# Kernel tuning notes

Hardware: AMD Instinct MI355X
Metric: run time of the kernel (lower is better)

The kernel has to match this reference:

```python
import jax, jax.numpy as jnp
import numpy as np

K = 3       # kernel_size
RATE = 2    # dilation rate
NH = 8      # num_heads
EPS = 1e-5  # InstanceNorm eps


def _conv1x1(x, W, b):
    # x: [B,C,H,W], W: [O,C], b: [O]
    return jnp.einsum('bchw,oc->bohw', x, W) + b[None, :, None, None]


def _inorm(x):
    mu = jnp.mean(x, axis=(2, 3), keepdims=True)
    var = jnp.var(x, axis=(2, 3), keepdims=True)
    return (x - mu) / jnp.sqrt(var + EPS)


def _extract_patches(x):
    # dilated KxK patches, stride 1, 'same' grid -> [B, C, K*K, H, W]
    B, C, H, W = x.shape
    pad = RATE * (K - 1) // 2
    xp = jnp.pad(x, ((0, 0), (0, 0), (pad, pad), (pad, pad)))
    taps = [xp[:, :, i * RATE:i * RATE + H, j * RATE:j * RATE + W]
            for i in range(K) for j in range(K)]
    return jnp.stack(taps, axis=2)


def setup_inputs() -> dict:
    key = jax.random.key(0)
    ks = jax.random.split(key, 8)
    B, C, H, W, A = 1, 64, 64, 64, 128
    features = jax.random.normal(ks[0], (B, C, H, W), jnp.float32)
    masks = jax.random.uniform(ks[1], (B, 1, H, W), jnp.float32)
    s_in = 1.0 / np.sqrt(C).astype(np.float32)
    Wq = jax.random.normal(ks[2], (A, C), jnp.float32) * s_in
    bq = jnp.zeros((A,), jnp.float32)
    Wk = jax.random.normal(ks[3], (A, C), jnp.float32) * s_in
    bk = jnp.zeros((A,), jnp.float32)
    Wo = jax.random.normal(ks[4], (C, C), jnp.float32) * s_in
    bo = jnp.zeros((C,), jnp.float32)
    return dict(features=features, masks=masks, Wq=Wq, bq=bq,
                Wk=Wk, bk=bk, Wo=Wo, bo=bo)


def reference(features, masks, Wq, bq, Wk, bk, Wo, bo):
    B, C, H, W = features.shape
    A = Wq.shape[0]
    hc = A // NH
    L = H * W
    KK = K * K

    m = (masks > 0.5).astype(features.dtype)          # 1 = hole
    f_masked = features * m
    f_unmasked = features * (1.0 - m)

    q = jax.nn.relu(_inorm(_conv1x1(f_masked, Wq, bq)))    # [B,A,H,W]
    k = jax.nn.relu(_inorm(_conv1x1(f_unmasked, Wk, bk)))  # [B,A,H,W]

    # per-head dilated patch banks: [B,NH,hc*KK,L]
    qp = _extract_patches(q).reshape(B, NH, hc * KK, L)
    kp = _extract_patches(k).reshape(B, NH, hc * KK, L)

    # patch-correlation attention per head: [B,NH,L,L]
    attn = jax.nn.softmax(jnp.einsum('bndq,bndk->bnqk', qp, kp), axis=-1)

    # value patch bank from unmasked features: [B,C*KK,L]
    vp = _extract_patches(f_unmasked).reshape(B, C * KK, L)

    # sample value patches: [B,NH,L,C*KK]
    sampled = jnp.einsum('bnqk,bdk->bnqd', attn, vp)

    # fold: average the KK taps per channel, then average over heads
    attended = sampled.reshape(B, NH, L, C, KK).mean(axis=4).mean(axis=1)  # [B,L,C]
    attended = attended.transpose(0, 2, 1).reshape(B, C, H, W)

    return jax.nn.relu(_inorm(_conv1x1(attended, Wo, bo)))
```

## Files before the change

kernel.cpp:

```cpp
#include <hip/hip_runtime.h>
#include <hip/hip_bf16.h>


#define LL 4096
#define CC 64
#define AA 128
#define NH_ 8
#define KSTR 144
#define LOG2E 1.44269504088896340736f

typedef _Float16 half8 __attribute__((ext_vector_type(8)));
typedef float floatx4 __attribute__((ext_vector_type(4)));
typedef int intx4 __attribute__((ext_vector_type(4)));

__device__ __forceinline__ float fexp2(float x) {
    float r;
    asm("v_exp_f32 %0, %1" : "=v"(r) : "v"(x));
    return r;
}

__global__ __launch_bounds__(256) void prep_kernel(
    const float* __restrict__ feat,
    const float* __restrict__ masks,
    const float* __restrict__ Wq, const float* __restrict__ bq,
    const float* __restrict__ Wk, const float* __restrict__ bk,
    _Float16* __restrict__ q_act, _Float16* __restrict__ k_act,
    _Float16* __restrict__ vb)
{
    const int tid = threadIdx.x;
    const int b = blockIdx.x;
    __shared__ float sW[CC];
    __shared__ float sm[8];

    if (b >= 2 * AA) {
        int c = b - 2 * AA;
        for (int p = 0; p < 16; ++p) {
            int l = p * 256 + tid;
            int y = l >> 6, x = l & 63;
            float s = 0.f;
            for (int ty = 0; ty < 3; ++ty) {
                int yy = y + 2 * (ty - 1);
                if (yy < 0 || yy > 63) continue;
                for (int tx = 0; tx < 3; ++tx) {
                    int xx = x + 2 * (tx - 1);
                    if (xx < 0 || xx > 63) continue;
                    int ll = yy * 64 + xx;
                    float hole = masks[ll] > 0.5f ? 1.f : 0.f;
                    s += feat[c * LL + ll] * (1.f - hole);
                }
            }
            vb[c * LL + l] = (_Float16)(s * (1.f / 9.f));
        }
        return;
    }

    const int a = b & (AA - 1);
    const int sel = b >> 7;
    const float* Wrow = (sel ? Wk : Wq) + a * CC;
    const float bias = sel ? bk[a] : bq[a];
    if (tid < CC) sW[tid] = Wrow[tid];
    __syncthreads();

    float acc[16];
#pragma unroll
    for (int p = 0; p < 16; ++p) acc[p] = 0.f;
    for (int c = 0; c < CC; ++c) {
        float wc = sW[c];
        const float* fr = feat + (size_t)c * LL + tid;
#pragma unroll
        for (int p = 0; p < 16; ++p) acc[p] += wc * fr[p * 256];
    }

    float vals[16];
    float s1 = 0.f, s2 = 0.f;
#pragma unroll
    for (int p = 0; p < 16; ++p) {
        int l = p * 256 + tid;
        float hole = masks[l] > 0.5f ? 1.f : 0.f;
        float mf = sel ? (1.f - hole) : hole;
        float v = acc[p] * mf + bias;
        vals[p] = v; s1 += v; s2 += v * v;
    }
    for (int off = 32; off; off >>= 1) {
        s1 += __shfl_down(s1, off, 64);
        s2 += __shfl_down(s2, off, 64);
    }
    int wv = tid >> 6, ln = tid & 63;
    if (ln == 0) { sm[wv * 2] = s1; sm[wv * 2 + 1] = s2; }
    __syncthreads();
    s1 = sm[0] + sm[2] + sm[4] + sm[6];
    s2 = sm[1] + sm[3] + sm[5] + sm[7];
    float mu = s1 * (1.f / LL);
    float inv = rsqrtf(s2 * (1.f / LL) - mu * mu + 1e-5f);

    const float oscale = sel ? 1.f : LOG2E;
    _Float16* act = (sel ? k_act : q_act) + (size_t)a * LL;
#pragma unroll
    for (int p = 0; p < 16; ++p) {
        int l = p * 256 + tid;
        float v = (vals[p] - mu) * inv;
        act[l] = (_Float16)(v > 0.f ? v * oscale : 0.f);
    }
}

__global__ __launch_bounds__(256) void build_kp(
    const _Float16* __restrict__ k_act, _Float16* __restrict__ kp)
{
    const int n = blockIdx.x, y = blockIdx.y;
    const int tid = threadIdx.x;
    const _Float16* ka = k_act + (size_t)n * 16 * LL;
    _Float16* base = kp + ((size_t)n * LL + y * 64) * KSTR;
#pragma unroll
    for (int i = 0; i < 5; ++i) {
        int idx = tid + i * 256;
        if (idx < 64 * 18) {
            int x = idx / 18, c18 = idx - x * 18;
            half8 v8;
#pragma unroll
            for (int j = 0; j < 8; ++j) {
                int d = c18 * 8 + j;
                int ah = d / 9, t = d - ah * 9;
                int ty = t / 3, tx = t - ty * 3;
                int yy = y + 2 * (ty - 1);
                int xx = x + 2 * (tx - 1);
                _Float16 v = (_Float16)0.f;
                if (yy >= 0 && yy <= 63 && xx >= 0 && xx <= 63)
                    v = ka[ah * LL + yy * 64 + xx];
                v8[j] = v;
            }
            *(half8*)(base + (size_t)idx * 8) = v8;
        }
    }
}

__global__ __launch_bounds__(256, 2) void attn_kernel(
    const _Float16* __restrict__ q_act, const _Float16* __restrict__ kp,
    const _Float16* __restrict__ vb,
    _Float16* __restrict__ Opart, float* __restrict__ ml)
{
    const int qt2 = blockIdx.x, n = blockIdx.y, h = blockIdx.z;
    const int jt0 = h * 32;
    const int tid = threadIdx.x;
    const int w = tid >> 6, lane = tid & 63;
    const int l15 = lane & 15, quad = lane >> 4;

    __shared__ __align__(16) _Float16 Bk[2][64 * KSTR + 16];
    __shared__ __align__(16) _Float16 Vt[2][64 * 64];

    if (tid < 32) Bk[tid >> 4][64 * KSTR + (tid & 15)] = (_Float16)0.f;

    const _Float16* kpn = kp + (size_t)n * LL * KSTR;
    const uint4* vbu = (const uint4*)vb;

    const int vc0 = tid >> 3, ve0 = tid & 7;
    const int vc1 = vc0 + 32, ve1 = ve0;
    const int vs0 = vc0 * 8 + (ve0 ^ (vc0 & 7));
    const int vs1 = vc1 * 8 + (ve1 ^ (vc1 & 7));

    auto issue_bk = [&](int jt, _Float16* dst) {
        const char* tile = (const char*)(kpn + (size_t)jt * 64 * KSTR) + (lane << 4);
        for (int c = w; c < 18; c += 4) {
            __builtin_amdgcn_global_load_lds(
                (const __attribute__((address_space(1))) void*)(tile + c * 1024),
                (__attribute__((address_space(3))) void*)(dst + c * 512),
                16, 0, 0);
        }
    };

    half8 afrag[2][5];
    {
        const _Float16* qa = q_act + (size_t)n * 16 * LL;
        const int x = w * 16 + l15;
#pragma unroll
        for (int rs = 0; rs < 2; ++rs) {
            const int y = qt2 * 2 + rs;
#pragma unroll
            for (int ks = 0; ks < 5; ++ks) {
#pragma unroll
                for (int j = 0; j < 8; ++j) {
                    int d = ks * 32 + quad * 8 + j;
                    _Float16 v = (_Float16)0.f;
                    if (d < 144) {
                        int ah = d / 9, t = d - ah * 9;
                        int ty = t / 3, tx = t - ty * 3;
                        int yy = y + 2 * (ty - 1);
                        int xx = x + 2 * (tx - 1);
                        if (yy >= 0 && yy <= 63 && xx >= 0 && xx <= 63)
                            v = qa[ah * LL + yy * 64 + xx];
                    }
                    afrag[rs][ks][j] = v;
                }
            }
        }
    }

    floatx4 accO[2][4];
    float mrow[2], lrow[2];
#pragma unroll
    for (int rs = 0; rs < 2; ++rs) {
        mrow[rs] = -1e30f; lrow[rs] = 0.f;
#pragma unroll
        for (int i = 0; i < 4; ++i) accO[rs][i] = (floatx4){0.f, 0.f, 0.f, 0.f};
    }

    const int aLo = (((quad & 1) << 5) + l15) << 2;
    const int aHi = aLo + 64;
    const bool selHi = (quad >> 1) != 0;

    uint4 vreg[2];
    issue_bk(jt0, Bk[0]);
    vreg[0] = vbu[vc0 * (LL / 8) + jt0 * 8 + ve0];
    vreg[1] = vbu[vc1 * (LL / 8) + jt0 * 8 + ve1];

    int cur = 0;
    for (int it = 0; it < 32; ++it) {
        {
            uint4* vd = (uint4*)Vt[cur];
            vd[vs0] = vreg[0];
            vd[vs1] = vreg[1];
        }

        __syncthreads();

        if (it < 31) {
            const int jn = jt0 + it + 1;
            issue_bk(jn, Bk[cur ^ 1]);
            vreg[0] = vbu[vc0 * (LL / 8) + jn * 8 + ve0];
            vreg[1] = vbu[vc1 * (LL / 8) + jn * 8 + ve1];
        }

        const _Float16* bk = Bk[cur];
        const _Float16* vt = Vt[cur];

        floatx4 accS[2][4];
#pragma unroll
        for (int rs = 0; rs < 2; ++rs)
#pragma unroll
            for (int i = 0; i < 4; ++i) accS[rs][i] = (floatx4){0.f, 0.f, 0.f, 0.f};
        __builtin_amdgcn_s_setprio(1);
        for (int ks = 0; ks < 5; ++ks) {
#pragma unroll
            for (int nt = 0; nt < 4; ++nt) {
                half8 bfr = *(const half8*)(bk + (nt * 16 + l15) * KSTR + ks * 32 + quad * 8);
                accS[0][nt] = __builtin_amdgcn_mfma_f32_16x16x32_f16(bfr, afrag[0][ks], accS[0][nt], 0, 0, 0);
                accS[1][nt] = __builtin_amdgcn_mfma_f32_16x16x32_f16(bfr, afrag[1][ks], accS[1][nt], 0, 0, 0);
            }
        }
        __builtin_amdgcn_s_setprio(0);

        half8 pfr[2][2];
#pragma unroll
        for (int rs = 0; rs < 2; ++rs) {
            float t0 = fmaxf(fmaxf(accS[rs][0][0], accS[rs][0][1]), fmaxf(accS[rs][0][2], accS[rs][0][3]));
            float t1 = fmaxf(fmaxf(accS[rs][1][0], accS[rs][1][1]), fmaxf(accS[rs][1][2], accS[rs][1][3]));
            float t2 = fmaxf(fmaxf(accS[rs][2][0], accS[rs][2][1]), fmaxf(accS[rs][2][2], accS[rs][2][3]));
            float t3 = fmaxf(fmaxf(accS[rs][3][0], accS[rs][3][1]), fmaxf(accS[rs][3][2], accS[rs][3][3]));
            float tm = fmaxf(fmaxf(t0, t1), fmaxf(t2, t3));
            if (!__all(tm <= mrow[rs] + 3.0f)) {
                tm = fmaxf(tm, __shfl_xor(tm, 16, 64));
                tm = fmaxf(tm, __shfl_xor(tm, 32, 64));
                float mn = fmaxf(mrow[rs], tm);
                float alpha = fexp2(mrow[rs] - mn);
                mrow[rs] = mn;
                lrow[rs] *= alpha;
                float af[4];
#pragma unroll
                for (int r = 0; r < 4; ++r) af[r] = __shfl(alpha, quad * 4 + r, 16);
#pragma unroll
                for (int nt = 0; nt < 4; ++nt)
#pragma unroll
                    for (int r = 0; r < 4; ++r) accO[rs][nt][r] *= af[r];
            }
            float rsum = 0.f;
#pragma unroll
            for (int nt = 0; nt < 4; ++nt)
#pragma unroll
                for (int r = 0; r < 4; ++r) {
                    float pv = fexp2(accS[rs][nt][r] - mrow[rs]);
                    accS[rs][nt][r] = pv;
                    rsum += pv;
                }
            lrow[rs] += rsum;

            int pkw[4][2];
#pragma unroll
            for (int nt = 0; nt < 4; ++nt)
#pragma unroll
                for (int rp = 0; rp < 2; ++rp) {
                    auto hp = __builtin_amdgcn_cvt_pkrtz(accS[rs][nt][2 * rp],
                                                         accS[rs][nt][2 * rp + 1]);
                    pkw[nt][rp] = __builtin_bit_cast(int, hp);
                }
#pragma unroll
            for (int ks2 = 0; ks2 < 2; ++ks2) {
                int w0A = __builtin_amdgcn_ds_bpermute(aLo, pkw[2 * ks2][0]);
                int w0B = __builtin_amdgcn_ds_bpermute(aLo, pkw[2 * ks2 + 1][0]);
                int w1A = __builtin_amdgcn_ds_bpermute(aLo, pkw[2 * ks2][1]);
                int w1B = __builtin_amdgcn_ds_bpermute(aLo, pkw[2 * ks2 + 1][1]);
                int w2A = __builtin_amdgcn_ds_bpermute(aHi, pkw[2 * ks2][0]);
                int w2B = __builtin_amdgcn_ds_bpermute(aHi, pkw[2 * ks2 + 1][0]);
                int w3A = __builtin_amdgcn_ds_bpermute(aHi, pkw[2 * ks2][1]);
                int w3B = __builtin_amdgcn_ds_bpermute(aHi, pkw[2 * ks2 + 1][1]);
                intx4 wvv;
                wvv[0] = selHi ? w0B : w0A;
                wvv[1] = selHi ? w1B : w1A;
                wvv[2] = selHi ? w2B : w2A;
                wvv[3] = selHi ? w3B : w3A;
                pfr[rs][ks2] = __builtin_bit_cast(half8, wvv);
            }
        }

        __builtin_amdgcn_s_setprio(1);
#pragma unroll
        for (int ks2 = 0; ks2 < 2; ++ks2) {
#pragma unroll
            for (int nt = 0; nt < 4; ++nt) {
                half8 bfr = *(const half8*)(vt + (nt * 16 + l15) * 64 +
                                            (((ks2 * 4 + quad) ^ (l15 & 7)) << 3));
                accO[0][nt] = __builtin_amdgcn_mfma_f32_16x16x32_f16(pfr[0][ks2], bfr, accO[0][nt], 0, 0, 0);
                accO[1][nt] = __builtin_amdgcn_mfma_f32_16x16x32_f16(pfr[1][ks2], bfr, accO[1][nt], 0, 0, 0);
            }
        }
        __builtin_amdgcn_s_setprio(0);

        cur ^= 1;
    }

#pragma unroll
    for (int rs = 0; rs < 2; ++rs) {
        const int y = qt2 * 2 + rs;
        float rsum = lrow[rs];
        rsum += __shfl_xor(rsum, 16, 64);
        rsum += __shfl_xor(rsum, 32, 64);
        float invl = 1.f / rsum;
        float iv[4];
#pragma unroll
        for (int r = 0; r < 4; ++r) iv[r] = __shfl(invl, quad * 4 + r, 16);

        _Float16* op = Opart + ((size_t)(n * 2 + h) * LL + y * 64 + w * 16) * CC;
#pragma unroll
        for (int r = 0; r < 4; ++r)
#pragma unroll
            for (int nt = 0; nt < 4; ++nt)
                op[(quad * 4 + r) * CC + nt * 16 + l15] = (_Float16)(accO[rs][nt][r] * iv[r]);

        if (quad == 0) {
            float* mlp = ml + ((size_t)n * LL + y * 64 + w * 16 + l15) * 4;
            mlp[2 * h] = mrow[rs];
            mlp[2 * h + 1] = rsum;
        }
    }
}

__global__ __launch_bounds__(256) void combine_kernel(
    const _Float16* __restrict__ Opart, const float* __restrict__ ml,
    float* __restrict__ att)
{
    int t = blockIdx.x * 256 + threadIdx.x;
    int l = t >> 6, c = t & 63;
    float s = 0.f;
#pragma unroll
    for (int n = 0; n < NH_; ++n) {
        const float* mlp = ml + ((size_t)n * LL + l) * 4;
        float m0 = mlp[0], l0 = mlp[1], m1 = mlp[2], l1 = mlp[3];
        float M = fmaxf(m0, m1);
        float w0 = l0 * fexp2(m0 - M);
        float w1 = l1 * fexp2(m1 - M);
        float o0 = (float)Opart[((size_t)(2 * n) * LL + l) * CC + c];
        float o1 = (float)Opart[((size_t)(2 * n + 1) * LL + l) * CC + c];
        s += (w0 * o0 + w1 * o1) / (w0 + w1);
    }
    att[t] = s * 0.125f;
}

__global__ __launch_bounds__(256) void out_kernel(
    const float* __restrict__ att,
    const float* __restrict__ Wo, const float* __restrict__ bo,
    float* __restrict__ out)
{
    const int o = blockIdx.x;
    const int tid = threadIdx.x;
    __shared__ float sW[CC];
    __shared__ float sm[8];
    if (tid < CC) sW[tid] = Wo[o * CC + tid];
    __syncthreads();
    const float bias = bo[o];

    float vals[16], s1 = 0.f, s2 = 0.f;
    for (int p = 0; p < 16; ++p) {
        int l = p * 256 + tid;
        const float4* arow = (const float4*)(att + (size_t)l * CC);
        float acc = bias;
#pragma unroll
        for (int c4 = 0; c4 < 16; ++c4) {
            float4 a4 = arow[c4];
            acc += sW[c4 * 4] * a4.x + sW[c4 * 4 + 1] * a4.y +
                   sW[c4 * 4 + 2] * a4.z + sW[c4 * 4 + 3] * a4.w;
        }
        vals[p] = acc; s1 += acc; s2 += acc * acc;
    }
    for (int off = 32; off; off >>= 1) {
        s1 += __shfl_down(s1, off, 64);
        s2 += __shfl_down(s2, off, 64);
    }
    int wv = tid >> 6, ln = tid & 63;
    if (ln == 0) { sm[wv * 2] = s1; sm[wv * 2 + 1] = s2; }
    __syncthreads();
    s1 = sm[0] + sm[2] + sm[4] + sm[6];
    s2 = sm[1] + sm[3] + sm[5] + sm[7];
    float mu = s1 * (1.f / LL);
    float inv = rsqrtf(s2 * (1.f / LL) - mu * mu + 1e-5f);
    for (int p = 0; p < 16; ++p) {
        int l = p * 256 + tid;
        float v = (vals[p] - mu) * inv;
        out[(size_t)o * LL + l] = v > 0.f ? v : 0.f;
    }
}

extern "C" void kernel_launch(void* const* d_in, const int* in_sizes, int n_in,
                              void* d_out, int out_size, void* d_ws, size_t ws_size,
                              hipStream_t stream) {
    const float* feat  = (const float*)d_in[0];
    const float* masks = (const float*)d_in[1];
    const float* Wq    = (const float*)d_in[2];
    const float* bq    = (const float*)d_in[3];
    const float* Wk    = (const float*)d_in[4];
    const float* bk    = (const float*)d_in[5];
    const float* Wo    = (const float*)d_in[6];
    const float* bo    = (const float*)d_in[7];
    float* out = (float*)d_out;

    char* ws = (char*)d_ws;
    _Float16* q_act = (_Float16*)ws;
    _Float16* k_act = (_Float16*)(ws + 1048576);
    _Float16* vb    = (_Float16*)(ws + 2097152);
    float*    att   = (float*)(ws + 2621440);
    _Float16* kp    = (_Float16*)(ws + 3670016);
    _Float16* Opart = (_Float16*)(ws + 13107200);
    float*    ml    = (float*)(ws + 21495808);

    prep_kernel<<<2 * AA + CC, 256, 0, stream>>>(feat, masks, Wq, bq, Wk, bk,
                                                 q_act, k_act, vb);
    dim3 gb(NH_, 64);
    build_kp<<<gb, 256, 0, stream>>>(k_act, kp);
    dim3 g(32, NH_, 2);
    attn_kernel<<<g, 256, 0, stream>>>(q_act, kp, vb, Opart, ml);
    combine_kernel<<<LL * CC / 256, 256, 0, stream>>>(Opart, ml, att);
    out_kernel<<<CC, 256, 0, stream>>>(att, Wo, bo, out);
}
```

Measured before the change: 232.4 us.

## Load V fragments directly from global memory and flatten grid for head-major ordering

The V tile is no longer staged through shared memory. Each lane loads its MFMA B-operand fragments straight from global (L2-resident) memory, which removes the LDS stores, the swizzle and the LDS reads, and halves the shared-memory footprint. The grid is flattened to 1D with the head index innermost, so blocks sharing the same query tile and V slice are scheduled together for cache reuse. The cost is that the V loads are issued inside the loop, where they may stall the PV MFMAs on global latency, and the accesses are 16-byte strided loads across rows.

```diff
diff --git a/kernel.cpp b/kernel.cpp
--- a/kernel.cpp
+++ b/kernel.cpp
@@ -138,24 +138,21 @@
     const _Float16* __restrict__ vb,
     _Float16* __restrict__ Opart, float* __restrict__ ml)
 {
-    const int qt2 = blockIdx.x, n = blockIdx.y, h = blockIdx.z;
+    const int bid = blockIdx.x;
+    const int n = bid & 7;
+    const int slot = bid >> 3;
+    const int qt2 = slot & 31;
+    const int h = slot >> 5;
     const int jt0 = h * 32;
     const int tid = threadIdx.x;
     const int w = tid >> 6, lane = tid & 63;
     const int l15 = lane & 15, quad = lane >> 4;
 
     __shared__ __align__(16) _Float16 Bk[2][64 * KSTR + 16];
-    __shared__ __align__(16) _Float16 Vt[2][64 * 64];
 
     if (tid < 32) Bk[tid >> 4][64 * KSTR + (tid & 15)] = (_Float16)0.f;
 
     const _Float16* kpn = kp + (size_t)n * LL * KSTR;
-    const uint4* vbu = (const uint4*)vb;
-
-    const int vc0 = tid >> 3, ve0 = tid & 7;
-    const int vc1 = vc0 + 32, ve1 = ve0;
-    const int vs0 = vc0 * 8 + (ve0 ^ (vc0 & 7));
-    const int vs1 = vc1 * 8 + (ve1 ^ (vc1 & 7));
 
     auto issue_bk = [&](int jt, _Float16* dst) {
         const char* tile = (const char*)(kpn + (size_t)jt * 64 * KSTR) + (lane << 4);
@@ -207,30 +204,25 @@
     const int aHi = aLo + 64;
     const bool selHi = (quad >> 1) != 0;
 
-    uint4 vreg[2];
+    const _Float16* vpl = vb + (size_t)l15 * LL + quad * 8;
+
     issue_bk(jt0, Bk[0]);
-    vreg[0] = vbu[vc0 * (LL / 8) + jt0 * 8 + ve0];
-    vreg[1] = vbu[vc1 * (LL / 8) + jt0 * 8 + ve1];
 
     int cur = 0;
     for (int it = 0; it < 32; ++it) {
-        {
-            uint4* vd = (uint4*)Vt[cur];
-            vd[vs0] = vreg[0];
-            vd[vs1] = vreg[1];
-        }
-
         __syncthreads();
 
-        if (it < 31) {
-            const int jn = jt0 + it + 1;
-            issue_bk(jn, Bk[cur ^ 1]);
-            vreg[0] = vbu[vc0 * (LL / 8) + jn * 8 + ve0];
-            vreg[1] = vbu[vc1 * (LL / 8) + jn * 8 + ve1];
-        }
+        if (it < 31) issue_bk(jt0 + it + 1, Bk[cur ^ 1]);
+
+        const _Float16* vp = vpl + (jt0 + it) * 64;
+        half8 vfrag[4][2];
+#pragma unroll
+        for (int nt = 0; nt < 4; ++nt)
+#pragma unroll
+            for (int ks2 = 0; ks2 < 2; ++ks2)
+                vfrag[nt][ks2] = *(const half8*)(vp + (size_t)nt * 16 * LL + ks2 * 32);
 
         const _Float16* bk = Bk[cur];
-        const _Float16* vt = Vt[cur];
 
         floatx4 accS[2][4];
 #pragma unroll
@@ -315,10 +307,8 @@
         for (int ks2 = 0; ks2 < 2; ++ks2) {
 #pragma unroll
             for (int nt = 0; nt < 4; ++nt) {
-                half8 bfr = *(const half8*)(vt + (nt * 16 + l15) * 64 +
-                                            (((ks2 * 4 + quad) ^ (l15 & 7)) << 3));
-                accO[0][nt] = __builtin_amdgcn_mfma_f32_16x16x32_f16(pfr[0][ks2], bfr, accO[0][nt], 0, 0, 0);
-                accO[1][nt] = __builtin_amdgcn_mfma_f32_16x16x32_f16(pfr[1][ks2], bfr, accO[1][nt], 0, 0, 0);
+                accO[0][nt] = __builtin_amdgcn_mfma_f32_16x16x32_f16(pfr[0][ks2], vfrag[nt][ks2], accO[0][nt], 0, 0, 0);
+                accO[1][nt] = __builtin_amdgcn_mfma_f32_16x16x32_f16(pfr[1][ks2], vfrag[nt][ks2], accO[1][nt], 0, 0, 0);
             }
         }
         __builtin_amdgcn_s_setprio(0);
@@ -443,8 +433,7 @@
                                                  q_act, k_act, vb);
     dim3 gb(NH_, 64);
     build_kp<<<gb, 256, 0, stream>>>(k_act, kp);
-    dim3 g(32, NH_, 2);
-    attn_kernel<<<g, 256, 0, stream>>>(q_act, kp, vb, Opart, ml);
+    attn_kernel<<<512, 256, 0, stream>>>(q_act, kp, vb, Opart, ml);
     combine_kernel<<<LL * CC / 256, 256, 0, stream>>>(Opart, ml, att);
     out_kernel<<<CC, 256, 0, stream>>>(att, Wo, bo, out);
 }
```

Result: no change. 232.5 us (+0.1%).
